# Optimization experiments

Hardware: AMD Instinct MI355X
Metric: run time of the kernel (lower is better)

## Reference

```python
import jax, jax.numpy as jnp
import numpy as np

B, T, IN, H, OUT = 256, 100, 128, 1024, 35
BITS = 4
SLOPE = 25.0
THR_H = 1.0
THR_O = 1.0
BETA1, BETA2, BETA3, BETA4 = 0.9, 0.85, 0.8, 0.95


def fake_quant(w, w_min, w_max, bits=BITS):
    # FakeQuantize in training mode: STE -> forward value is quantized, grad passes through clamp
    levels = 2 ** bits
    scale = (w_max - w_min) / (levels - 1)
    wc = jnp.clip(w, w_min, w_max)
    q = jnp.round((wc - w_min) / scale) * scale + w_min
    return wc + jax.lax.stop_gradient(q - wc)


@jax.custom_vjp
def spike(x):
    # Heaviside forward, fast-sigmoid surrogate backward (snn.surrogate.fast_sigmoid)
    return (x > 0).astype(x.dtype)

def _spike_fwd(x):
    return (x > 0).astype(x.dtype), x

def _spike_bwd(x, g):
    return (g / (SLOPE * jnp.abs(x) + 1.0) ** 2,)

spike.defvjp(_spike_fwd, _spike_bwd)


def lif_step(cur, mem, beta, thr, reset_mechanism):
    # snntorch Leaky (reset_delay semantics): reset computed from previous mem, detached
    reset = jax.lax.stop_gradient((mem > thr).astype(cur.dtype))
    base = beta * mem + cur
    if reset_mechanism == "subtract":
        mem_new = base - reset * thr
    else:  # "zero"
        mem_new = base - reset * base
    spk = spike(mem_new - thr)
    return spk, mem_new


def setup_inputs() -> dict:
    key = jax.random.key(0)
    ks = jax.random.split(key, 5)
    x = jax.random.normal(ks[0], (B, T, IN), dtype=jnp.float32)
    # QuantLinear init: uniform(w_min, w_max); fc1 uses (-0.5, 0.5), others (0.001, 1.0)
    w1 = jax.random.uniform(ks[1], (H, IN), minval=-0.5, maxval=0.5, dtype=jnp.float32)
    w2 = jax.random.uniform(ks[2], (H, H), minval=0.001, maxval=1.0, dtype=jnp.float32)
    w3 = jax.random.uniform(ks[3], (H, H), minval=0.001, maxval=1.0, dtype=jnp.float32)
    w4 = jax.random.uniform(ks[4], (OUT, H), minval=0.001, maxval=1.0, dtype=jnp.float32)
    return {"x": x, "w1": w1, "w2": w2, "w3": w3, "w4": w4}


def reference(x, w1, w2, w3, w4):
    # hoist weight quantization out of the time loop (identical math each step)
    q1 = fake_quant(w1, -0.5, 0.5)
    q2 = fake_quant(w2, 0.001, 1.0)
    q3 = fake_quant(w3, 0.001, 1.0)
    q4 = fake_quant(w4, 0.001, 1.0)
    xs = jnp.transpose(x, (1, 0, 2)) / 15.0  # [T, B, IN]
    Bx = x.shape[0]

    def step(carry, xt):
        m1, m2, m3, m4 = carry
        s1, m1 = lif_step(xt @ q1.T, m1, BETA1, THR_H, "subtract")
        s2, m2 = lif_step(s1 @ q2.T, m2, BETA2, THR_H, "subtract")
        s3, m3 = lif_step(s2 @ q3.T, m3, BETA3, THR_H, "subtract")
        s4, m4 = lif_step(s3 @ q4.T, m4, BETA4, THR_O, "zero")
        return (m1, m2, m3, m4), (s1, s2, s3, s4, m4)

    init = (jnp.zeros((Bx, H), x.dtype), jnp.zeros((Bx, H), x.dtype),
            jnp.zeros((Bx, H), x.dtype), jnp.zeros((Bx, OUT), x.dtype))
    _, (spk1, spk2, spk3, spk4, mem4) = jax.lax.scan(step, init, xs)
    # stacked along time dim 0, matching torch.stack(dim=0)
    return spk1, spk2, spk3, spk4, mem4
```

## Files before the change

kernel.cpp:

```cpp
#include <hip/hip_runtime.h>
#include <stdint.h>

#define NB  256
#define NT  100
#define NIN 128
#define NH  1024
#define NOUT 35

#define O_SPK2 26214400ull
#define O_SPK3 52428800ull
#define O_SPK4 78643200ull
#define O_MEM4 79539200ull

#define WS_XT   0ull
#define WS_Q1T  13107200ull
#define WS_K2T  13631488ull
#define WS_K3T  14680064ull
#define WS_K4T  15728640ull
#define WS_RS2  15777792ull
#define WS_RS3  15781888ull
#define WS_RS4  15785984ull

#define S2C ((float)((1.0 - 0.001) / 15.0))
#define S1C ((float)(1.0 / 15.0))

__global__ void k_prep(const float* __restrict__ x, const float* __restrict__ w1,
                       const float* __restrict__ w2, const float* __restrict__ w3,
                       const float* __restrict__ w4, uint8_t* __restrict__ ws)
{
  long long id = (long long)blockIdx.x * 256 + threadIdx.x;
  if (id < 1048576) {
    int i = (int)(id >> 10), j = (int)(id & 1023);
    float wv = w2[(size_t)j * 1024 + i];
    float wc = fminf(fmaxf(wv, 0.001f), 1.0f);
    ws[WS_K2T + id] = (uint8_t)(int)rintf((wc - 0.001f) / S2C);
    return;
  }
  id -= 1048576;
  if (id < 1048576) {
    int i = (int)(id >> 10), j = (int)(id & 1023);
    float wv = w3[(size_t)j * 1024 + i];
    float wc = fminf(fmaxf(wv, 0.001f), 1.0f);
    ws[WS_K3T + id] = (uint8_t)(int)rintf((wc - 0.001f) / S2C);
    return;
  }
  id -= 1048576;
  if (id < 49152) {
    int i = (int)(id / 48), j = (int)(id % 48);
    uint8_t v = 0;
    if (j < NOUT) {
      float wv = w4[(size_t)j * 1024 + i];
      float wc = fminf(fmaxf(wv, 0.001f), 1.0f);
      v = (uint8_t)(int)rintf((wc - 0.001f) / S2C);
    }
    ws[WS_K4T + id] = v;
    return;
  }
  id -= 49152;
  if (id < 131072) {
    int i = (int)(id >> 10), j = (int)(id & 1023);
    float wv = w1[(size_t)j * 128 + i];
    float wc = fminf(fmaxf(wv, -0.5f), 0.5f);
    float q = rintf((wc + 0.5f) / S1C) * S1C - 0.5f;
    ((float*)(ws + WS_Q1T))[id] = q;
    return;
  }
  id -= 131072;
  if (id < 3276800) {
    int row = (int)(id >> 7), i = (int)(id & 127);
    int tt = row >> 8, bb = row & 255;
    ((float*)(ws + WS_XT))[id] = x[((size_t)bb * NT + tt) * NIN + i] / 15.0f;
  }
}

__global__ void k_rowsum(const float* __restrict__ w2, const float* __restrict__ w3,
                         const float* __restrict__ w4, uint8_t* __restrict__ ws)
{
  int bid = blockIdx.x, tid = threadIdx.x;
  const float* W;
  uint32_t* o;
  if (bid < 1024)      { W = w2 + (size_t)bid * 1024;          o = (uint32_t*)(ws + WS_RS2) + bid; }
  else if (bid < 2048) { W = w3 + (size_t)(bid - 1024) * 1024; o = (uint32_t*)(ws + WS_RS3) + (bid - 1024); }
  else                 { W = w4 + (size_t)(bid - 2048) * 1024; o = (uint32_t*)(ws + WS_RS4) + (bid - 2048); }
  uint32_t s = 0;
  for (int i = tid; i < 1024; i += 256) {
    float wc = fminf(fmaxf(W[i], 0.001f), 1.0f);
    s += (uint32_t)(int)rintf((wc - 0.001f) / S2C);
  }
  #pragma unroll
  for (int off = 32; off; off >>= 1) s += (uint32_t)__shfl_down((int)s, off);
  __shared__ uint32_t red[4];
  if ((tid & 63) == 0) red[tid >> 6] = s;
  __syncthreads();
  if (tid == 0) *o = red[0] + red[1] + red[2] + red[3];
}

__global__ __launch_bounds__(256) void k_cur1(const uint8_t* __restrict__ ws, float* __restrict__ out)
{
  __shared__ float xsT[128 * 68];
  __shared__ float qch[16 * 256];
  const float* xt  = (const float*)(ws + WS_XT);
  const float* q1T = (const float*)(ws + WS_Q1T);
  const int tid = threadIdx.x;
  const int rb = blockIdx.x >> 2, cb = blockIdx.x & 3;
  const int jI = tid & 63, rI = tid >> 6;
  const int j4 = jI * 4, r16 = rI * 16;

  #pragma unroll
  for (int k = 0; k < 32; ++k) {
    int e = tid + k * 256;
    int r = e >> 7, i = e & 127;
    xsT[i * 68 + r] = xt[((size_t)rb * 64 + r) * 128 + i];
  }
  float acc[16][4];
  #pragma unroll
  for (int d = 0; d < 16; ++d) {
    acc[d][0] = 0.f; acc[d][1] = 0.f; acc[d][2] = 0.f; acc[d][3] = 0.f;
  }
  for (int ic = 0; ic < 8; ++ic) {
    __syncthreads();
    #pragma unroll
    for (int k = 0; k < 16; ++k) {
      int e = tid + k * 256;
      int ii = e >> 8, j = e & 255;
      qch[ii * 256 + j] = q1T[((size_t)(ic * 16 + ii) << 10) + cb * 256 + j];
    }
    __syncthreads();
    #pragma unroll
    for (int ii = 0; ii < 16; ++ii) {
      int i = ic * 16 + ii;
      const float4 q  = *(const float4*)&qch[ii * 256 + j4];
      const float4 xa = *(const float4*)&xsT[i * 68 + r16];
      const float4 xb = *(const float4*)&xsT[i * 68 + r16 + 4];
      const float4 xc = *(const float4*)&xsT[i * 68 + r16 + 8];
      const float4 xd = *(const float4*)&xsT[i * 68 + r16 + 12];
      float xr[16];
      xr[0]=xa.x; xr[1]=xa.y; xr[2]=xa.z; xr[3]=xa.w;
      xr[4]=xb.x; xr[5]=xb.y; xr[6]=xb.z; xr[7]=xb.w;
      xr[8]=xc.x; xr[9]=xc.y; xr[10]=xc.z; xr[11]=xc.w;
      xr[12]=xd.x; xr[13]=xd.y; xr[14]=xd.z; xr[15]=xd.w;
      #pragma unroll
      for (int d = 0; d < 16; ++d) {
        acc[d][0] = fmaf(xr[d], q.x, acc[d][0]);
        acc[d][1] = fmaf(xr[d], q.y, acc[d][1]);
        acc[d][2] = fmaf(xr[d], q.z, acc[d][2]);
        acc[d][3] = fmaf(xr[d], q.w, acc[d][3]);
      }
    }
  }
  #pragma unroll
  for (int d = 0; d < 16; ++d) {
    float4 v = make_float4(acc[d][0], acc[d][1], acc[d][2], acc[d][3]);
    *(float4*)&out[((size_t)rb * 64 + r16 + d) * 1024 + cb * 256 + j4] = v;
  }
}

__global__ __launch_bounds__(512) void k_main(const uint8_t* __restrict__ ws, float* out)
{
  const int b = blockIdx.x;
  const int tid = threadIdx.x;
  const int lane = tid & 63;
  const int wave = tid >> 6;
  const int g8 = wave;
  const int n64 = lane;

  const uint8_t* k2T = ws + WS_K2T;
  const uint8_t* k3T = ws + WS_K3T;
  const uint8_t* k4T = ws + WS_K4T;
  const uint32_t* rs2 = (const uint32_t*)(ws + WS_RS2);
  const uint32_t* rs3 = (const uint32_t*)(ws + WS_RS3);
  const uint32_t* rs4 = (const uint32_t*)(ws + WS_RS4);

  __shared__ uint16_t list[1024];
  __shared__ uint32_t pEa[2048];
  __shared__ uint32_t pOa[2048];
  __shared__ uint32_t wcnt[8];
  __shared__ uint32_t lpos;

  float m1[2] = {0.f, 0.f}, m2[2] = {0.f, 0.f}, m3[2] = {0.f, 0.f}, m4 = 0.f;
  uint32_t r2[2], r3[2], r4v = 0;
  r2[0] = rs2[tid]; r2[1] = rs2[tid + 512];
  r3[0] = rs3[tid]; r3[1] = rs3[tid + 512];
  if (tid < NOUT) r4v = rs4[tid];

  uint32_t nT, nL; bool cm;
  auto buildList = [&](bool sA, bool sB) {
    if (tid == 0) lpos = 0;
    uint64_t bA = __ballot(sA), bB = __ballot(sB);
    if (lane == 0) wcnt[wave] = (uint32_t)(__popcll(bA) + __popcll(bB));
    __syncthreads();
    nT = wcnt[0]+wcnt[1]+wcnt[2]+wcnt[3]+wcnt[4]+wcnt[5]+wcnt[6]+wcnt[7];
    cm = nT > 512;
    nL = cm ? (1024u - nT) : nT;
    uint64_t cA = cm ? ~bA : bA;
    uint64_t cB = cm ? ~bB : bB;
    uint32_t cnt = (uint32_t)(__popcll(cA) + __popcll(cB));
    uint32_t bs = 0;
    if (lane == 0) bs = atomicAdd(&lpos, cnt);
    bs = (uint32_t)__shfl((int)bs, 0);
    uint64_t ltm = (1ull << lane) - 1ull;
    if ((cA >> lane) & 1ull) list[bs + (uint32_t)__popcll(cA & ltm)] = (uint16_t)tid;
    if ((cB >> lane) & 1ull) list[bs + (uint32_t)__popcll(cA) + (uint32_t)__popcll(cB & ltm)] = (uint16_t)(tid + 512);
    __syncthreads();
  };

  auto gatherBig = [&](const uint8_t* mat) {
    uint32_t aE0=0,aE1=0,aE2=0,aE3=0,aO0=0,aO1=0,aO2=0,aO3=0;
    const uint8_t* bp = mat + (n64 << 4);
    for (uint32_t a = (uint32_t)g8; a < nL; a += 8) {
      uint32_t idx = list[a];
      const uint4 w = *(const uint4*)(bp + ((size_t)idx << 10));
      aE0 += w.x & 0x00FF00FFu; aO0 += (w.x >> 8) & 0x00FF00FFu;
      aE1 += w.y & 0x00FF00FFu; aO1 += (w.y >> 8) & 0x00FF00FFu;
      aE2 += w.z & 0x00FF00FFu; aO2 += (w.z >> 8) & 0x00FF00FFu;
      aE3 += w.w & 0x00FF00FFu; aO3 += (w.w >> 8) & 0x00FF00FFu;
    }
    int basei = (g8 << 8) + (n64 << 2);
    pEa[basei+0]=aE0; pEa[basei+1]=aE1; pEa[basei+2]=aE2; pEa[basei+3]=aE3;
    pOa[basei+0]=aO0; pOa[basei+1]=aO1; pOa[basei+2]=aO2; pOa[basei+3]=aO3;
  };

  auto gsum = [&](int j) -> uint32_t {
    int w = j >> 2;
    int sh = (j & 2) << 3;
    const uint32_t* P = (j & 1) ? pOa : pEa;
    uint32_t s = 0;
    #pragma unroll
    for (int gg = 0; gg < 8; ++gg) s += (P[(gg << 8) + w] >> sh) & 0xffffu;
    return s;
  };

  float curN[2];
  {
    size_t row0 = (size_t)b * NH;
    curN[0] = out[row0 + tid];
    curN[1] = out[row0 + tid + 512];
  }

  for (int t = 0; t < NT; ++t) {
    const size_t rowH = ((size_t)t * NB + b) * (size_t)NH;
    const size_t rowO = ((size_t)t * NB + b) * (size_t)NOUT;
    bool sA, sB;
    {
      float c0 = curN[0], c1 = curN[1];
      int tn = (t + 1 < NT) ? (t + 1) : t;
      size_t rowN = ((size_t)tn * NB + b) * (size_t)NH;
      curN[0] = out[rowN + tid];
      curN[1] = out[rowN + tid + 512];
      float rst0 = m1[0] > 1.0f ? 1.0f : 0.0f;
      m1[0] = fmaf(0.9f, m1[0], c0) - rst0;
      sA = (m1[0] - 1.0f) > 0.0f;
      out[rowH + tid] = sA ? 1.0f : 0.0f;
      float rst1 = m1[1] > 1.0f ? 1.0f : 0.0f;
      m1[1] = fmaf(0.9f, m1[1], c1) - rst1;
      sB = (m1[1] - 1.0f) > 0.0f;
      out[rowH + tid + 512] = sB ? 1.0f : 0.0f;
    }
    buildList(sA, sB);
    uint32_t n1 = nT, nl1 = nL; bool cm1 = cm;
    if (nl1) gatherBig(k2T);
    __syncthreads();
    {
      float nb = 0.001f * (float)n1;
      #pragma unroll
      for (int c = 0; c < 2; ++c) {
        int j = (c << 9) + tid;
        uint32_t gsv = nl1 ? gsum(j) : 0u;
        uint32_t K = cm1 ? (r2[c] - gsv) : gsv;
        float cur = fmaf(S2C, (float)K, nb);
        float rst = m2[c] > 1.0f ? 1.0f : 0.0f;
        m2[c] = fmaf(0.85f, m2[c], cur) - rst;
        bool sp = (m2[c] - 1.0f) > 0.0f;
        out[O_SPK2 + rowH + j] = sp ? 1.0f : 0.0f;
        if (c == 0) sA = sp; else sB = sp;
      }
    }
    buildList(sA, sB);
    uint32_t n2 = nT, nl2 = nL; bool cm2 = cm;
    if (nl2) gatherBig(k3T);
    __syncthreads();
    {
      float nb = 0.001f * (float)n2;
      #pragma unroll
      for (int c = 0; c < 2; ++c) {
        int j = (c << 9) + tid;
        uint32_t gsv = nl2 ? gsum(j) : 0u;
        uint32_t K = cm2 ? (r3[c] - gsv) : gsv;
        float cur = fmaf(S2C, (float)K, nb);
        float rst = m3[c] > 1.0f ? 1.0f : 0.0f;
        m3[c] = fmaf(0.8f, m3[c], cur) - rst;
        bool sp = (m3[c] - 1.0f) > 0.0f;
        out[O_SPK3 + rowH + j] = sp ? 1.0f : 0.0f;
        if (c == 0) sA = sp; else sB = sp;
      }
    }
    buildList(sA, sB);
    uint32_t n3 = nT, nl3 = nL; bool cm3 = cm;
    if (nl3 && n64 < 3) {
      uint32_t aE0=0,aE1=0,aE2=0,aE3=0,aO0=0,aO1=0,aO2=0,aO3=0;
      const uint8_t* bp = k4T + (n64 << 4);
      for (uint32_t a = (uint32_t)g8; a < nl3; a += 8) {
        uint32_t idx = list[a];
        const uint4 w = *(const uint4*)(bp + (size_t)idx * 48);
        aE0 += w.x & 0x00FF00FFu; aO0 += (w.x >> 8) & 0x00FF00FFu;
        aE1 += w.y & 0x00FF00FFu; aO1 += (w.y >> 8) & 0x00FF00FFu;
        aE2 += w.z & 0x00FF00FFu; aO2 += (w.z >> 8) & 0x00FF00FFu;
        aE3 += w.w & 0x00FF00FFu; aO3 += (w.w >> 8) & 0x00FF00FFu;
      }
      int basei = (g8 << 8) + (n64 << 2);
      pEa[basei+0]=aE0; pEa[basei+1]=aE1; pEa[basei+2]=aE2; pEa[basei+3]=aE3;
      pOa[basei+0]=aO0; pOa[basei+1]=aO1; pOa[basei+2]=aO2; pOa[basei+3]=aO3;
    }
    __syncthreads();
    if (tid < NOUT) {
      uint32_t gsv = nl3 ? gsum(tid) : 0u;
      uint32_t K = cm3 ? (r4v - gsv) : gsv;
      float cur = fmaf(S2C, (float)K, 0.001f * (float)n3);
      float rst = m4 > 1.0f ? 1.0f : 0.0f;
      float bsv = fmaf(0.95f, m4, cur);
      m4 = (rst > 0.0f) ? 0.0f : bsv;
      out[O_SPK4 + rowO + tid] = ((m4 - 1.0f) > 0.0f) ? 1.0f : 0.0f;
      out[O_MEM4 + rowO + tid] = m4;
    }
  }
}

extern "C" void kernel_launch(void* const* d_in, const int* in_sizes, int n_in,
                              void* d_out, int out_size, void* d_ws, size_t ws_size,
                              hipStream_t stream)
{
  const float* x  = (const float*)d_in[0];
  const float* w1 = (const float*)d_in[1];
  const float* w2 = (const float*)d_in[2];
  const float* w3 = (const float*)d_in[3];
  const float* w4 = (const float*)d_in[4];
  float* out = (float*)d_out;
  uint8_t* ws = (uint8_t*)d_ws;
  hipLaunchKernelGGL(k_prep,   dim3(21696), dim3(256), 0, stream, x, w1, w2, w3, w4, ws);
  hipLaunchKernelGGL(k_rowsum, dim3(2083),  dim3(256), 0, stream, w2, w3, w4, ws);
  hipLaunchKernelGGL(k_cur1,   dim3(1600),  dim3(256), 0, stream, ws, out);
  hipLaunchKernelGGL(k_main,   dim3(256),   dim3(512), 0, stream, ws, out);
}
```

Measured before the change: 683.6 us.

## Fuse layer-1 LIF into per-batch spk1 kernel and widen main kernel to 1024 threads

Replaces the tiled layer-1 GEMM kernel with a per-batch kernel that computes the input current and runs the layer-1 LIF recurrence in one place, writing spikes directly. The main recurrent kernel no longer does the layer-1 LIF step and just reads the precomputed spikes. The main kernel moves from 512 to 1024 threads, one neuron per thread, with 16 waves sharing the sparse gather. The gather loop is also unrolled by two and uses readfirstlane for the row index. The spk1 kernel reads x through uncoalesced, wave-uniform global loads and has only 256 blocks with no LDS tiling, so its GEMM may be less efficient than the old tiled version. Doubling the main kernel's threads adds cross-wave reduction work and may raise register pressure.

```diff
diff --git a/kernel.cpp b/kernel.cpp
--- a/kernel.cpp
+++ b/kernel.cpp
@@ -95,223 +95,199 @@
   if (tid == 0) *o = red[0] + red[1] + red[2] + red[3];
 }
 
-__global__ __launch_bounds__(256) void k_cur1(const uint8_t* __restrict__ ws, float* __restrict__ out)
-{
-  __shared__ float xsT[128 * 68];
-  __shared__ float qch[16 * 256];
-  const float* xt  = (const float*)(ws + WS_XT);
-  const float* q1T = (const float*)(ws + WS_Q1T);
-  const int tid = threadIdx.x;
-  const int rb = blockIdx.x >> 2, cb = blockIdx.x & 3;
-  const int jI = tid & 63, rI = tid >> 6;
-  const int j4 = jI * 4, r16 = rI * 16;
-
-  #pragma unroll
-  for (int k = 0; k < 32; ++k) {
-    int e = tid + k * 256;
-    int r = e >> 7, i = e & 127;
-    xsT[i * 68 + r] = xt[((size_t)rb * 64 + r) * 128 + i];
-  }
-  float acc[16][4];
-  #pragma unroll
-  for (int d = 0; d < 16; ++d) {
-    acc[d][0] = 0.f; acc[d][1] = 0.f; acc[d][2] = 0.f; acc[d][3] = 0.f;
-  }
-  for (int ic = 0; ic < 8; ++ic) {
-    __syncthreads();
+__global__ __launch_bounds__(1024, 1) void k_spk1(const float* __restrict__ xt,
+                                                  const float* __restrict__ q1T,
+                                                  float* __restrict__ out)
+{
+  const int b = blockIdx.x;
+  const int j = threadIdx.x;
+  float m1 = 0.f;
+  for (int c = 0; c < 4; ++c) {
+    float acc[25];
     #pragma unroll
-    for (int k = 0; k < 16; ++k) {
-      int e = tid + k * 256;
-      int ii = e >> 8, j = e & 255;
-      qch[ii * 256 + j] = q1T[((size_t)(ic * 16 + ii) << 10) + cb * 256 + j];
-    }
-    __syncthreads();
+    for (int tt = 0; tt < 25; ++tt) acc[tt] = 0.f;
+    #pragma unroll 2
+    for (int ib = 0; ib < 16; ++ib) {
+      float q[8];
+      #pragma unroll
+      for (int u = 0; u < 8; ++u) q[u] = q1T[(size_t)(ib * 8 + u) * NH + j];
+      #pragma unroll
+      for (int tt = 0; tt < 25; ++tt) {
+        const float* xr = xt + ((size_t)(c * 25 + tt) * NB + b) * NIN + ib * 8;
+        #pragma unroll
+        for (int u = 0; u < 8; ++u) acc[tt] = fmaf(xr[u], q[u], acc[tt]);
+      }
+    }
     #pragma unroll
-    for (int ii = 0; ii < 16; ++ii) {
-      int i = ic * 16 + ii;
-      const float4 q  = *(const float4*)&qch[ii * 256 + j4];
-      const float4 xa = *(const float4*)&xsT[i * 68 + r16];
-      const float4 xb = *(const float4*)&xsT[i * 68 + r16 + 4];
-      const float4 xc = *(const float4*)&xsT[i * 68 + r16 + 8];
-      const float4 xd = *(const float4*)&xsT[i * 68 + r16 + 12];
-      float xr[16];
-      xr[0]=xa.x; xr[1]=xa.y; xr[2]=xa.z; xr[3]=xa.w;
-      xr[4]=xb.x; xr[5]=xb.y; xr[6]=xb.z; xr[7]=xb.w;
-      xr[8]=xc.x; xr[9]=xc.y; xr[10]=xc.z; xr[11]=xc.w;
-      xr[12]=xd.x; xr[13]=xd.y; xr[14]=xd.z; xr[15]=xd.w;
-      #pragma unroll
-      for (int d = 0; d < 16; ++d) {
-        acc[d][0] = fmaf(xr[d], q.x, acc[d][0]);
-        acc[d][1] = fmaf(xr[d], q.y, acc[d][1]);
-        acc[d][2] = fmaf(xr[d], q.z, acc[d][2]);
-        acc[d][3] = fmaf(xr[d], q.w, acc[d][3]);
-      }
-    }
-  }
-  #pragma unroll
-  for (int d = 0; d < 16; ++d) {
-    float4 v = make_float4(acc[d][0], acc[d][1], acc[d][2], acc[d][3]);
-    *(float4*)&out[((size_t)rb * 64 + r16 + d) * 1024 + cb * 256 + j4] = v;
-  }
-}
-
-__global__ __launch_bounds__(512) void k_main(const uint8_t* __restrict__ ws, float* out)
+    for (int tt = 0; tt < 25; ++tt) {
+      const int t = c * 25 + tt;
+      float rst = m1 > 1.0f ? 1.0f : 0.0f;
+      m1 = fmaf(0.9f, m1, acc[tt]) - rst;
+      bool sp = (m1 - 1.0f) > 0.0f;
+      out[((size_t)t * NB + b) * NH + j] = sp ? 1.0f : 0.0f;
+    }
+  }
+}
+
+__global__ __launch_bounds__(1024, 1) void k_main(
+    const uint8_t* __restrict__ k2T, const uint8_t* __restrict__ k3T,
+    const uint8_t* __restrict__ k4T, const uint32_t* __restrict__ rs2,
+    const uint32_t* __restrict__ rs3, const uint32_t* __restrict__ rs4,
+    float* __restrict__ out)
 {
   const int b = blockIdx.x;
   const int tid = threadIdx.x;
   const int lane = tid & 63;
   const int wave = tid >> 6;
-  const int g8 = wave;
-  const int n64 = lane;
-
-  const uint8_t* k2T = ws + WS_K2T;
-  const uint8_t* k3T = ws + WS_K3T;
-  const uint8_t* k4T = ws + WS_K4T;
-  const uint32_t* rs2 = (const uint32_t*)(ws + WS_RS2);
-  const uint32_t* rs3 = (const uint32_t*)(ws + WS_RS3);
-  const uint32_t* rs4 = (const uint32_t*)(ws + WS_RS4);
 
   __shared__ uint16_t list[1024];
-  __shared__ uint32_t pEa[2048];
-  __shared__ uint32_t pOa[2048];
-  __shared__ uint32_t wcnt[8];
+  __shared__ uint4    pEa4[1024];
+  __shared__ uint4    pOa4[1024];
+  __shared__ uint4    wcnt4[4];
   __shared__ uint32_t lpos;
-
-  float m1[2] = {0.f, 0.f}, m2[2] = {0.f, 0.f}, m3[2] = {0.f, 0.f}, m4 = 0.f;
-  uint32_t r2[2], r3[2], r4v = 0;
-  r2[0] = rs2[tid]; r2[1] = rs2[tid + 512];
-  r3[0] = rs3[tid]; r3[1] = rs3[tid + 512];
-  if (tid < NOUT) r4v = rs4[tid];
-
-  uint32_t nT, nL; bool cm;
-  auto buildList = [&](bool sA, bool sB) {
-    if (tid == 0) lpos = 0;
-    uint64_t bA = __ballot(sA), bB = __ballot(sB);
-    if (lane == 0) wcnt[wave] = (uint32_t)(__popcll(bA) + __popcll(bB));
-    __syncthreads();
-    nT = wcnt[0]+wcnt[1]+wcnt[2]+wcnt[3]+wcnt[4]+wcnt[5]+wcnt[6]+wcnt[7];
-    cm = nT > 512;
-    nL = cm ? (1024u - nT) : nT;
-    uint64_t cA = cm ? ~bA : bA;
-    uint64_t cB = cm ? ~bB : bB;
-    uint32_t cnt = (uint32_t)(__popcll(cA) + __popcll(cB));
+  uint32_t* pEa  = (uint32_t*)pEa4;
+  uint32_t* pOa  = (uint32_t*)pOa4;
+  uint32_t* wcnt = (uint32_t*)wcnt4;
+
+  float m2 = 0.f, m3 = 0.f, m4 = 0.f;
+  const uint32_t r2v = rs2[tid];
+  const uint32_t r3v = rs3[tid];
+  const uint32_t r4v = (tid < NOUT) ? rs4[tid] : 0u;
+
+  auto sumcnt = [&]() -> uint32_t {
+    uint4 a0 = wcnt4[0], a1 = wcnt4[1], a2 = wcnt4[2], a3 = wcnt4[3];
+    return a0.x + a0.y + a0.z + a0.w + a1.x + a1.y + a1.z + a1.w +
+           a2.x + a2.y + a2.z + a2.w + a3.x + a3.y + a3.z + a3.w;
+  };
+
+  auto writeList = [&](uint64_t cw) {
+    uint32_t cnt = (uint32_t)__popcll(cw);
     uint32_t bs = 0;
     if (lane == 0) bs = atomicAdd(&lpos, cnt);
     bs = (uint32_t)__shfl((int)bs, 0);
-    uint64_t ltm = (1ull << lane) - 1ull;
-    if ((cA >> lane) & 1ull) list[bs + (uint32_t)__popcll(cA & ltm)] = (uint16_t)tid;
-    if ((cB >> lane) & 1ull) list[bs + (uint32_t)__popcll(cA) + (uint32_t)__popcll(cB & ltm)] = (uint16_t)(tid + 512);
-    __syncthreads();
+    if ((cw >> lane) & 1ull)
+      list[bs + (uint32_t)__popcll(cw & ((1ull << lane) - 1ull))] = (uint16_t)tid;
   };
 
-  auto gatherBig = [&](const uint8_t* mat) {
+  auto gatherBig = [&](const uint8_t* __restrict__ mat, uint32_t nLv) {
     uint32_t aE0=0,aE1=0,aE2=0,aE3=0,aO0=0,aO1=0,aO2=0,aO3=0;
-    const uint8_t* bp = mat + (n64 << 4);
-    for (uint32_t a = (uint32_t)g8; a < nL; a += 8) {
-      uint32_t idx = list[a];
-      const uint4 w = *(const uint4*)(bp + ((size_t)idx << 10));
-      aE0 += w.x & 0x00FF00FFu; aO0 += (w.x >> 8) & 0x00FF00FFu;
-      aE1 += w.y & 0x00FF00FFu; aO1 += (w.y >> 8) & 0x00FF00FFu;
-      aE2 += w.z & 0x00FF00FFu; aO2 += (w.z >> 8) & 0x00FF00FFu;
-      aE3 += w.w & 0x00FF00FFu; aO3 += (w.w >> 8) & 0x00FF00FFu;
-    }
-    int basei = (g8 << 8) + (n64 << 2);
-    pEa[basei+0]=aE0; pEa[basei+1]=aE1; pEa[basei+2]=aE2; pEa[basei+3]=aE3;
-    pOa[basei+0]=aO0; pOa[basei+1]=aO1; pOa[basei+2]=aO2; pOa[basei+3]=aO3;
+    const uint8_t* bp = mat + (lane << 4);
+    uint32_t a = (uint32_t)wave;
+    for (; a + 16 < nLv; a += 32) {
+      uint32_t i0 = (uint32_t)__builtin_amdgcn_readfirstlane((int)list[a]);
+      uint32_t i1 = (uint32_t)__builtin_amdgcn_readfirstlane((int)list[a + 16]);
+      const uint4 w0 = *(const uint4*)(bp + ((size_t)i0 << 10));
+      const uint4 w1 = *(const uint4*)(bp + ((size_t)i1 << 10));
+      aE0 += w0.x & 0x00FF00FFu; aO0 += (w0.x >> 8) & 0x00FF00FFu;
+      aE1 += w0.y & 0x00FF00FFu; aO1 += (w0.y >> 8) & 0x00FF00FFu;
+      aE2 += w0.z & 0x00FF00FFu; aO2 += (w0.z >> 8) & 0x00FF00FFu;
+      aE3 += w0.w & 0x00FF00FFu; aO3 += (w0.w >> 8) & 0x00FF00FFu;
+      aE0 += w1.x & 0x00FF00FFu; aO0 += (w1.x >> 8) & 0x00FF00FFu;
+      aE1 += w1.y & 0x00FF00FFu; aO1 += (w1.y >> 8) & 0x00FF00FFu;
+      aE2 += w1.z & 0x00FF00FFu; aO2 += (w1.z >> 8) & 0x00FF00FFu;
+      aE3 += w1.w & 0x00FF00FFu; aO3 += (w1.w >> 8) & 0x00FF00FFu;
+    }
+    if (a < nLv) {
+      uint32_t i0 = (uint32_t)__builtin_amdgcn_readfirstlane((int)list[a]);
+      const uint4 w0 = *(const uint4*)(bp + ((size_t)i0 << 10));
+      aE0 += w0.x & 0x00FF00FFu; aO0 += (w0.x >> 8) & 0x00FF00FFu;
+      aE1 += w0.y & 0x00FF00FFu; aO1 += (w0.y >> 8) & 0x00FF00FFu;
+      aE2 += w0.z & 0x00FF00FFu; aO2 += (w0.z >> 8) & 0x00FF00FFu;
+      aE3 += w0.w & 0x00FF00FFu; aO3 += (w0.w >> 8) & 0x00FF00FFu;
+    }
+    const int basei = (wave << 8) + (lane << 2);
+    *(uint4*)&pEa[basei] = make_uint4(aE0, aE1, aE2, aE3);
+    *(uint4*)&pOa[basei] = make_uint4(aO0, aO1, aO2, aO3);
   };
 
-  auto gsum = [&](int j) -> uint32_t {
-    int w = j >> 2;
-    int sh = (j & 2) << 3;
-    const uint32_t* P = (j & 1) ? pOa : pEa;
+  auto gsum = [&](int jn) -> uint32_t {
+    int w = jn >> 2, sh = (jn & 2) << 3;
+    const uint32_t* P = (jn & 1) ? pOa : pEa;
     uint32_t s = 0;
     #pragma unroll
-    for (int gg = 0; gg < 8; ++gg) s += (P[(gg << 8) + w] >> sh) & 0xffffu;
+    for (int g = 0; g < 16; ++g) s += (P[(g << 8) + w] >> sh) & 0xffffu;
     return s;
   };
 
-  float curN[2];
-  {
-    size_t row0 = (size_t)b * NH;
-    curN[0] = out[row0 + tid];
-    curN[1] = out[row0 + tid + 512];
-  }
+  float s1v = out[(size_t)b * NH + tid];
+  uint32_t nT, nL; bool cm;
 
   for (int t = 0; t < NT; ++t) {
     const size_t rowH = ((size_t)t * NB + b) * (size_t)NH;
     const size_t rowO = ((size_t)t * NB + b) * (size_t)NOUT;
-    bool sA, sB;
+
+    bool sA = s1v > 0.5f;
     {
-      float c0 = curN[0], c1 = curN[1];
       int tn = (t + 1 < NT) ? (t + 1) : t;
-      size_t rowN = ((size_t)tn * NB + b) * (size_t)NH;
-      curN[0] = out[rowN + tid];
-      curN[1] = out[rowN + tid + 512];
-      float rst0 = m1[0] > 1.0f ? 1.0f : 0.0f;
-      m1[0] = fmaf(0.9f, m1[0], c0) - rst0;
-      sA = (m1[0] - 1.0f) > 0.0f;
-      out[rowH + tid] = sA ? 1.0f : 0.0f;
-      float rst1 = m1[1] > 1.0f ? 1.0f : 0.0f;
-      m1[1] = fmaf(0.9f, m1[1], c1) - rst1;
-      sB = (m1[1] - 1.0f) > 0.0f;
-      out[rowH + tid + 512] = sB ? 1.0f : 0.0f;
-    }
-    buildList(sA, sB);
-    uint32_t n1 = nT, nl1 = nL; bool cm1 = cm;
-    if (nl1) gatherBig(k2T);
-    __syncthreads();
+      s1v = out[((size_t)tn * NB + b) * (size_t)NH + tid];
+    }
+    uint64_t b1 = __ballot(sA);
+    if (tid == 0) lpos = 0;
+    if (lane == 0) wcnt[wave] = (uint32_t)__popcll(b1);
+    __syncthreads();
+    nT = sumcnt(); cm = nT > 512; nL = cm ? 1024u - nT : nT;
+    writeList(cm ? ~b1 : b1);
+    __syncthreads();
+    const uint32_t n1 = nT, nl1 = nL; const bool cm1 = cm;
+    if (nl1) gatherBig(k2T, nl1);
+    __syncthreads();
+
+    bool sp;
     {
-      float nb = 0.001f * (float)n1;
-      #pragma unroll
-      for (int c = 0; c < 2; ++c) {
-        int j = (c << 9) + tid;
-        uint32_t gsv = nl1 ? gsum(j) : 0u;
-        uint32_t K = cm1 ? (r2[c] - gsv) : gsv;
-        float cur = fmaf(S2C, (float)K, nb);
-        float rst = m2[c] > 1.0f ? 1.0f : 0.0f;
-        m2[c] = fmaf(0.85f, m2[c], cur) - rst;
-        bool sp = (m2[c] - 1.0f) > 0.0f;
-        out[O_SPK2 + rowH + j] = sp ? 1.0f : 0.0f;
-        if (c == 0) sA = sp; else sB = sp;
+      uint32_t gsv = nl1 ? gsum(tid) : 0u;
+      uint32_t K = cm1 ? (r2v - gsv) : gsv;
+      float cur = fmaf(S2C, (float)K, 0.001f * (float)n1);
+      float rst = m2 > 1.0f ? 1.0f : 0.0f;
+      m2 = fmaf(0.85f, m2, cur) - rst;
+      sp = (m2 - 1.0f) > 0.0f;
+      out[O_SPK2 + rowH + tid] = sp ? 1.0f : 0.0f;
+    }
+    uint64_t b2 = __ballot(sp);
+    if (tid == 0) lpos = 0;
+    if (lane == 0) wcnt[wave] = (uint32_t)__popcll(b2);
+    __syncthreads();
+    nT = sumcnt(); cm = nT > 512; nL = cm ? 1024u - nT : nT;
+    writeList(cm ? ~b2 : b2);
+    __syncthreads();
+    const uint32_t n2 = nT, nl2 = nL; const bool cm2 = cm;
+    if (nl2) gatherBig(k3T, nl2);
+    __syncthreads();
+
+    {
+      uint32_t gsv = nl2 ? gsum(tid) : 0u;
+      uint32_t K = cm2 ? (r3v - gsv) : gsv;
+      float cur = fmaf(S2C, (float)K, 0.001f * (float)n2);
+      float rst = m3 > 1.0f ? 1.0f : 0.0f;
+      m3 = fmaf(0.8f, m3, cur) - rst;
+      sp = (m3 - 1.0f) > 0.0f;
+      out[O_SPK3 + rowH + tid] = sp ? 1.0f : 0.0f;
+    }
+    uint64_t b3 = __ballot(sp);
+    if (tid == 0) lpos = 0;
+    if (lane == 0) wcnt[wave] = (uint32_t)__popcll(b3);
+    __syncthreads();
+    nT = sumcnt(); cm = nT > 512; nL = cm ? 1024u - nT : nT;
+    writeList(cm ? ~b3 : b3);
+    __syncthreads();
+    const uint32_t n3 = nT, nl3 = nL; const bool cm3 = cm;
+
+    if (nl3 && lane < 3) {
+      uint32_t aE0=0,aE1=0,aE2=0,aE3=0,aO0=0,aO1=0,aO2=0,aO3=0;
+      const uint8_t* bp = k4T + (lane << 4);
+      for (uint32_t a = (uint32_t)wave; a < nl3; a += 16) {
+        uint32_t i0 = (uint32_t)__builtin_amdgcn_readfirstlane((int)list[a]);
+        const uint4 w0 = *(const uint4*)(bp + (size_t)i0 * 48u);
+        aE0 += w0.x & 0x00FF00FFu; aO0 += (w0.x >> 8) & 0x00FF00FFu;
+        aE1 += w0.y & 0x00FF00FFu; aO1 += (w0.y >> 8) & 0x00FF00FFu;
+        aE2 += w0.z & 0x00FF00FFu; aO2 += (w0.z >> 8) & 0x00FF00FFu;
+        aE3 += w0.w & 0x00FF00FFu; aO3 += (w0.w >> 8) & 0x00FF00FFu;
       }
-    }
-    buildList(sA, sB);
-    uint32_t n2 = nT, nl2 = nL; bool cm2 = cm;
-    if (nl2) gatherBig(k3T);
-    __syncthreads();
-    {
-      float nb = 0.001f * (float)n2;
-      #pragma unroll
-      for (int c = 0; c < 2; ++c) {
-        int j = (c << 9) + tid;
-        uint32_t gsv = nl2 ? gsum(j) : 0u;
-        uint32_t K = cm2 ? (r3[c] - gsv) : gsv;
-        float cur = fmaf(S2C, (float)K, nb);
-        float rst = m3[c] > 1.0f ? 1.0f : 0.0f;
-        m3[c] = fmaf(0.8f, m3[c], cur) - rst;
-        bool sp = (m3[c] - 1.0f) > 0.0f;
-        out[O_SPK3 + rowH + j] = sp ? 1.0f : 0.0f;
-        if (c == 0) sA = sp; else sB = sp;
-      }
-    }
-    buildList(sA, sB);
-    uint32_t n3 = nT, nl3 = nL; bool cm3 = cm;
-    if (nl3 && n64 < 3) {
-      uint32_t aE0=0,aE1=0,aE2=0,aE3=0,aO0=0,aO1=0,aO2=0,aO3=0;
-      const uint8_t* bp = k4T + (n64 << 4);
-      for (uint32_t a = (uint32_t)g8; a < nl3; a += 8) {
-        uint32_t idx = list[a];
-        const uint4 w = *(const uint4*)(bp + (size_t)idx * 48);
-        aE0 += w.x & 0x00FF00FFu; aO0 += (w.x >> 8) & 0x00FF00FFu;
-        aE1 += w.y & 0x00FF00FFu; aO1 += (w.y >> 8) & 0x00FF00FFu;
-        aE2 += w.z & 0x00FF00FFu; aO2 += (w.z >> 8) & 0x00FF00FFu;
-        aE3 += w.w & 0x00FF00FFu; aO3 += (w.w >> 8) & 0x00FF00FFu;
-      }
-      int basei = (g8 << 8) + (n64 << 2);
-      pEa[basei+0]=aE0; pEa[basei+1]=aE1; pEa[basei+2]=aE2; pEa[basei+3]=aE3;
-      pOa[basei+0]=aO0; pOa[basei+1]=aO1; pOa[basei+2]=aO2; pOa[basei+3]=aO3;
-    }
-    __syncthreads();
+      const int basei = (wave << 8) + (lane << 2);
+      *(uint4*)&pEa[basei] = make_uint4(aE0, aE1, aE2, aE3);
+      *(uint4*)&pOa[basei] = make_uint4(aO0, aO1, aO2, aO3);
+    }
+    __syncthreads();
+
     if (tid < NOUT) {
       uint32_t gsv = nl3 ? gsum(tid) : 0u;
       uint32_t K = cm3 ? (r4v - gsv) : gsv;
@@ -338,6 +314,10 @@
   uint8_t* ws = (uint8_t*)d_ws;
   hipLaunchKernelGGL(k_prep,   dim3(21696), dim3(256), 0, stream, x, w1, w2, w3, w4, ws);
   hipLaunchKernelGGL(k_rowsum, dim3(2083),  dim3(256), 0, stream, w2, w3, w4, ws);
-  hipLaunchKernelGGL(k_cur1,   dim3(1600),  dim3(256), 0, stream, ws, out);
-  hipLaunchKernelGGL(k_main,   dim3(256),   dim3(512), 0, stream, ws, out);
-}
+  hipLaunchKernelGGL(k_spk1,   dim3(256),   dim3(1024), 0, stream,
+                     (const float*)(ws + WS_XT), (const float*)(ws + WS_Q1T), out);
+  hipLaunchKernelGGL(k_main,   dim3(256),   dim3(1024), 0, stream,
+                     ws + WS_K2T, ws + WS_K3T, ws + WS_K4T,
+                     (const uint32_t*)(ws + WS_RS2), (const uint32_t*)(ws + WS_RS3),
+                     (const uint32_t*)(ws + WS_RS4), out);
+}
```

New measurement: 883.0 us. 29.2% more time.
